# Performance work log

Measured on AMD Instinct MI355X. Metric: run time of the kernel, lower is better.

## Reference

```python
import jax, jax.numpy as jnp
import numpy as np

EMB = 256
ENT_NUM = 100000
REL_NUM = 2000
B = 512


def setup_inputs() -> dict:
    key = jax.random.key(0)
    ks = jax.random.split(key, 10)
    s = 0.02
    return {
        "left_child": jax.random.normal(ks[0], (B, 3, EMB), jnp.float32),
        "right_child": jax.random.normal(ks[1], (B, 3, EMB), jnp.float32),
        "query": jax.random.normal(ks[2], (B, 3, EMB), jnp.float32),
        "ent_emb": jax.random.normal(ks[3], (ENT_NUM, EMB), jnp.float32) * s,
        "rel_emb": jax.random.normal(ks[4], (REL_NUM, EMB), jnp.float32) * s,
        "W_left": jax.random.normal(ks[5], (EMB, EMB), jnp.float32) * s,
        "b_left": jnp.zeros((EMB,), jnp.float32),
        "W_right": jax.random.normal(ks[6], (EMB, EMB), jnp.float32) * s,
        "b_right": jnp.zeros((EMB,), jnp.float32),
        "W_ent": jax.random.normal(ks[7], (EMB, 3 * EMB), jnp.float32) * s,
        "b_ent": jnp.zeros((EMB,), jnp.float32),
    }


def _attend(q, table):
    # q: [B, E], table: [N, E]. Fused form of expand*mul*sum + softmax + expand*mul*sum.
    logits = q @ table.T                     # [B, N]
    probs = jax.nn.softmax(logits, axis=1)   # [B, N]
    return probs @ table                     # [B, E]


def reference(left_child, right_child, query, ent_emb, rel_emb,
              W_left, b_left, W_right, b_right, W_ent, b_ent):
    q1 = query[:, 1, :]
    left_rel = q1 @ W_left.T + b_left
    right_rel = q1 @ W_right.T + b_right
    # cat(query[:,0], query[:,1], query[:,2]) along dim 1 == reshape
    q_cat = query.reshape(query.shape[0], 3 * EMB)
    q_ent = q_cat @ W_ent.T + b_ent

    o_ent = _attend(q_ent, ent_emb)
    o_left_r = _attend(left_rel, rel_emb)
    o_right_r = _attend(right_rel, rel_emb)

    new_left = jnp.stack([left_child[:, 0, :], o_left_r, o_ent], axis=1)
    new_right = jnp.stack([o_ent, o_right_r, right_child[:, 2, :]], axis=1)
    return (new_left, new_right)
```

## Files before the change

kernel.cpp:

```cpp
#include <hip/hip_runtime.h>
#include <hip/hip_bf16.h>
#include <math.h>

typedef __bf16 bf16;
typedef unsigned short u16;
typedef unsigned int u32;
typedef unsigned long long u64;
typedef long long i64;
typedef unsigned char u8;
typedef __attribute__((ext_vector_type(8))) __bf16 bf16x8;
typedef __attribute__((ext_vector_type(16))) float f32x16;
typedef __attribute__((ext_vector_type(8))) int i32x8;
typedef __attribute__((address_space(1))) void gvoid;
typedef __attribute__((address_space(3))) void svoid;

#define ENT_N 100000
#define REL_N 2000
#define ENT_CH 120
#define REL_CH 4

#define NPREPM 1536
#define NCONV  6380
#define NCOPY  256

static __device__ __forceinline__ i32x8 mk8(uint4 a, uint4 b) {
    i32x8 r;
    r[0] = (int)a.x; r[1] = (int)a.y; r[2] = (int)a.z; r[3] = (int)a.w;
    r[4] = (int)b.x; r[5] = (int)b.y; r[6] = (int)b.z; r[7] = (int)b.w;
    return r;
}

template<int KLEN>
static __device__ __forceinline__ void prep_tile(
    const float* __restrict__ query, const float* __restrict__ W,
    const float* __restrict__ bias, int b0, int rowbase, int qwoff,
    bf16* __restrict__ outBf, u8* __restrict__ out8, float* smem)
{
    const int t = threadIdx.x;
    float* qs = smem;
    float* Wl = smem + 4 * KLEN;

#pragma unroll
    for (int i = 0; i < 4 * KLEN / 256; ++i) {
        const int l = t + 256 * i;
        const int r = l / KLEN, k = l % KLEN;
        qs[l] = query[(size_t)(b0 + r) * 768 + qwoff + k];
    }

    const int j = t & 63, r = t >> 6;
    float acc = 0.f;
    const float* wbase = W + (size_t)rowbase * KLEN;

    for (int c = 0; c < KLEN / 32; ++c) {
        __syncthreads();
#pragma unroll
        for (int p = 0; p < 2; ++p) {
            const int idx = t + p * 256;
            const int row = idx >> 3, kq = idx & 7;
            const float4 v = *(const float4*)(wbase + (size_t)row * KLEN + c * 32 + kq * 4);
            float* d = Wl + row * 33 + kq * 4;
            d[0] = v.x; d[1] = v.y; d[2] = v.z; d[3] = v.w;
        }
        __syncthreads();
        const float* wr = Wl + j * 33;
        const float* qr = qs + r * KLEN + c * 32;
#pragma unroll
        for (int k = 0; k < 32; ++k) acc += wr[k] * qr[k];
    }
    acc += bias[rowbase + j];

    const size_t o = (size_t)(b0 + r) * 256 + rowbase + j;
    outBf[o] = (bf16)acc;
    out8[o] = (u8)__builtin_amdgcn_cvt_pk_fp8_f32(acc, acc, 0, false);
}

__global__ __launch_bounds__(256) void prep_conv(
    const float* __restrict__ query,
    const float* __restrict__ W_left, const float* __restrict__ b_left,
    const float* __restrict__ W_right, const float* __restrict__ b_right,
    const float* __restrict__ W_ent, const float* __restrict__ b_ent,
    const float* __restrict__ lc, const float* __restrict__ rc,
    bf16* __restrict__ qe, bf16* __restrict__ ql, bf16* __restrict__ qr,
    u8* __restrict__ qe8, u8* __restrict__ ql8, u8* __restrict__ qr8,
    float* __restrict__ out,
    const float* __restrict__ entF, const float* __restrict__ relF,
    u8* __restrict__ entT, u8* __restrict__ entB,
    u8* __restrict__ relT, u8* __restrict__ relB,
    int nconv)
{
    __shared__ float smem[5184];
    const int blk = blockIdx.x;
    const int t = threadIdx.x;

    if (blk < NPREPM) {
        const int rg = blk / 12, jt = blk % 12;
        const int b0 = rg * 4;
        const int proj = jt >> 2, rowbase = (jt & 3) * 64;
        if (proj == 0)
            prep_tile<768>(query, W_ent, b_ent, b0, rowbase, 0, qe, qe8, smem);
        else if (proj == 1)
            prep_tile<256>(query, W_left, b_left, b0, rowbase, 256, ql, ql8, smem);
        else
            prep_tile<256>(query, W_right, b_right, b0, rowbase, 256, qr, qr8, smem);
        return;
    }
    if (blk >= NPREPM + nconv) {
        const int idx = (blk - NPREPM - nconv) * 256 + t;
        if (idx < 32768) {
            const int q = idx >> 6, e4 = idx & 63;
            float4 v = *(const float4*)(lc + (size_t)q * 768 + e4 * 4);
            *(float4*)(out + (size_t)q * 768 + e4 * 4) = v;
        } else {
            const int j = idx - 32768;
            const int q = j >> 6, e4 = j & 63;
            float4 v = *(const float4*)(rc + (size_t)q * 768 + 512 + e4 * 4);
            *(float4*)(out + (size_t)393216 + q * 768 + 512 + e4 * 4) = v;
        }
        return;
    }

    const int cidx = blk - NPREPM;
    const int x = cidx >> 2, y = cidx & 3;
    const float* in; u8* outT; u8* outB; int R; int g;
    if (x < 1563) {
        in = entF; outT = entT; outB = entB; R = ENT_N; g = x;
    } else {
        in = relF; outT = relT; outB = relB; R = REL_N; g = x - 1563;
    }
    const int r0 = g * 64;
    float* tile = smem;
    const int e0 = y * 64;

    const int eg = t & 7, rowb = t >> 3;
#pragma unroll
    for (int item = 0; item < 2; ++item) {
        const int r = rowb + item * 32;
        float4 a, b;
        if ((r0 + r) < R) {
            const float* src = in + (size_t)(r0 + r) * 256 + e0 + eg * 8;
            a = *(const float4*)src;
            b = *(const float4*)(src + 4);
        } else { a = make_float4(0.f, 0.f, 0.f, 0.f); b = a; }
        float* dst = tile + r * 65 + eg * 8;
        dst[0] = a.x; dst[1] = a.y; dst[2] = a.z; dst[3] = a.w;
        dst[4] = b.x; dst[5] = b.y; dst[6] = b.z; dst[7] = b.w;
    }
    __syncthreads();

    {
        const int n2 = t >> 2, piece = t & 3;
        const int sub = n2 >> 5, nn = n2 & 31;
        const int kbk = piece >> 1, jh = piece & 1;
        const float* src = tile + n2 * 65 + kbk * 32 + jh * 16;
        u32 xx; uint4 o;
        xx = __builtin_amdgcn_cvt_pk_fp8_f32(src[0], src[1], 0, false);
        o.x = __builtin_amdgcn_cvt_pk_fp8_f32(src[2], src[3], xx, true);
        xx = __builtin_amdgcn_cvt_pk_fp8_f32(src[4], src[5], 0, false);
        o.y = __builtin_amdgcn_cvt_pk_fp8_f32(src[6], src[7], xx, true);
        xx = __builtin_amdgcn_cvt_pk_fp8_f32(src[8], src[9], 0, false);
        o.z = __builtin_amdgcn_cvt_pk_fp8_f32(src[10], src[11], xx, true);
        xx = __builtin_amdgcn_cvt_pk_fp8_f32(src[12], src[13], 0, false);
        o.w = __builtin_amdgcn_cvt_pk_fp8_f32(src[14], src[15], xx, true);
        *(uint4*)(outB + (size_t)g * 16384 + sub * 8192 +
                  (size_t)y * 2048 + kbk * 1024 + nn * 32 + jh * 16) = o;
    }
    {
        const int etl = t >> 7, kbv = (t >> 6) & 1;
        const int nv = (t >> 1) & 31, jh = t & 1;
        const int colL = etl * 32 + nv;
        float v[16];
#pragma unroll
        for (int i = 0; i < 16; ++i) {
            const int row = jh * 32 + (i & 3) + 8 * (i >> 2) + 4 * kbv;
            v[i] = tile[row * 65 + colL];
        }
        u32 xx; uint4 o;
        xx = __builtin_amdgcn_cvt_pk_fp8_f32(v[0], v[1], 0, false);
        o.x = __builtin_amdgcn_cvt_pk_fp8_f32(v[2], v[3], xx, true);
        xx = __builtin_amdgcn_cvt_pk_fp8_f32(v[4], v[5], 0, false);
        o.y = __builtin_amdgcn_cvt_pk_fp8_f32(v[6], v[7], xx, true);
        xx = __builtin_amdgcn_cvt_pk_fp8_f32(v[8], v[9], 0, false);
        o.z = __builtin_amdgcn_cvt_pk_fp8_f32(v[10], v[11], xx, true);
        xx = __builtin_amdgcn_cvt_pk_fp8_f32(v[12], v[13], 0, false);
        o.w = __builtin_amdgcn_cvt_pk_fp8_f32(v[14], v[15], xx, true);
        *(uint4*)(outT + (size_t)g * 16384 +
                  (size_t)(y * 2 + etl) * 2048 +
                  kbv * 1024 + nv * 32 + jh * 16) = o;
    }
}

__global__ __launch_bounds__(256, 2) void flash10(
    const u8* __restrict__ qeP, const u8* __restrict__ qlP,
    const u8* __restrict__ qrP,
    const u8* __restrict__ entB, const u8* __restrict__ relB,
    const u8* __restrict__ entT, const u8* __restrict__ relT,
    float* __restrict__ entL, float* __restrict__ relLL,
    float* __restrict__ relLR,
    u16* __restrict__ entO, u16* __restrict__ relOL, u16* __restrict__ relOR)
{
    const int tid = threadIdx.x;
    const int w = tid >> 6;
    const int lane = tid & 63;
    const int n = lane & 31;
    const int kb = lane >> 5;

    int qt, c, stride, nt, Nrows;
    const u8* qbf; const u8* tabB; const u8* tabT;
    float* pL; u16* pO;
    {
        const int id = blockIdx.x;
        if (id < 480) {
            qt = id / 120; c = id % 120;
            stride = 120; nt = (c < 3) ? 14 : 13;
            Nrows = ENT_N;
            qbf = qeP; tabB = entB; tabT = entT; pL = entL; pO = entO;
        } else {
            const int r = id - 480;
            qt = (r >> 2) & 3; c = r & 3;
            stride = 4; nt = 8;
            Nrows = REL_N;
            tabB = relB; tabT = relT;
            if (r < 16) { qbf = qlP; pL = relLL; pO = relOL; }
            else        { qbf = qrP; pL = relLR; pO = relOR; }
        }
    }
    const int q0 = qt * 128;
    const int qw = q0 + w * 32;

    __shared__ __align__(16) u8 lds[65536];
    u16* lds16 = (u16*)lds;

    const u8* qrow = qbf + (size_t)(qw + n) * 256;
    i32x8 qf[4];
#pragma unroll
    for (int kc = 0; kc < 4; ++kc) {
        uint4 a = *(const uint4*)(qrow + kc * 64 + kb * 32);
        uint4 b = *(const uint4*)(qrow + kc * 64 + kb * 32 + 16);
        qf[kc] = mk8(a, b);
    }

    f32x16 acc[8];
#pragma unroll
    for (int et = 0; et < 8; ++et)
#pragma unroll
        for (int i = 0; i < 16; ++i) acc[et][i] = 0.f;
    float l_run = 0.f;

    auto stage = [&](int buf, int g) {
        u8* sK = lds + buf * 32768;
        u8* sV = sK + 16384;
        const u8* ksrc = tabB + (size_t)g * 16384 + w * 4096 + (size_t)lane * 16;
        const u8* vsrc = tabT + (size_t)g * 16384 + w * 4096 + (size_t)lane * 16;
#pragma unroll
        for (int o = 0; o < 4096; o += 1024) {
            __builtin_amdgcn_global_load_lds((gvoid*)(ksrc + o),
                                             (svoid*)(sK + w * 4096 + o), 16, 0, 0);
            __builtin_amdgcn_global_load_lds((gvoid*)(vsrc + o),
                                             (svoid*)(sV + w * 4096 + o), 16, 0, 0);
        }
    };

    int rt = c;
    stage(0, rt);
    __syncthreads();

    for (int k = 0; k < nt; ++k) {
        if (k + 1 < nt) stage((k + 1) & 1, rt + stride);

        const u8* sK = lds + (k & 1) * 32768;
        const u8* sV = sK + 16384;
        const int gr = rt * 64;

        f32x16 L0, L1;
#pragma unroll
        for (int i = 0; i < 16; ++i) { L0[i] = 0.f; L1[i] = 0.f; }
        const u8* kbase = sK + kb * 1024 + n * 32;
#pragma unroll
        for (int kc = 0; kc < 4; ++kc) {
            uint4 a0 = *(const uint4*)(kbase + kc * 2048);
            uint4 a1 = *(const uint4*)(kbase + kc * 2048 + 16);
            L0 = __builtin_amdgcn_mfma_scale_f32_32x32x64_f8f6f4(
                mk8(a0, a1), qf[kc], L0, 0, 0, 0, 0x7f7f7f7f, 0, 0x7f7f7f7f);
            uint4 b0 = *(const uint4*)(kbase + 8192 + kc * 2048);
            uint4 b1 = *(const uint4*)(kbase + 8192 + kc * 2048 + 16);
            L1 = __builtin_amdgcn_mfma_scale_f32_32x32x64_f8f6f4(
                mk8(b0, b1), qf[kc], L1, 0, 0, 0, 0x7f7f7f7f, 0, 0x7f7f7f7f);
        }
        if (gr + 64 > Nrows) {
#pragma unroll
            for (int r = 0; r < 16; ++r) {
                const int row = (r & 3) + 8 * (r >> 2) + 4 * kb;
                if (gr + row >= Nrows)      L0[r] = -1e30f;
                if (gr + 32 + row >= Nrows) L1[r] = -1e30f;
            }
        }
        float rs = 0.f;
#pragma unroll
        for (int r = 0; r < 16; ++r) {
            const float p0 = __expf(L0[r]); L0[r] = p0; rs += p0;
            const float p1 = __expf(L1[r]); L1[r] = p1; rs += p1;
        }
        rs += __shfl_xor(rs, 32);
        l_run += rs;
        u32 p[8];
#pragma unroll
        for (int i = 0; i < 4; ++i) {
            u32 x = __builtin_amdgcn_cvt_pk_fp8_f32(L0[i * 4 + 0], L0[i * 4 + 1], 0, false);
            p[i] = __builtin_amdgcn_cvt_pk_fp8_f32(L0[i * 4 + 2], L0[i * 4 + 3], x, true);
            u32 y = __builtin_amdgcn_cvt_pk_fp8_f32(L1[i * 4 + 0], L1[i * 4 + 1], 0, false);
            p[i + 4] = __builtin_amdgcn_cvt_pk_fp8_f32(L1[i * 4 + 2], L1[i * 4 + 3], y, true);
        }
        uint4 pa; pa.x = p[0]; pa.y = p[1]; pa.z = p[2]; pa.w = p[3];
        uint4 pb; pb.x = p[4]; pb.y = p[5]; pb.z = p[6]; pb.w = p[7];
        const i32x8 bv = mk8(pa, pb);
        const u8* vbase = sV + kb * 1024 + n * 32;
#pragma unroll
        for (int et = 0; et < 8; ++et) {
            uint4 v0 = *(const uint4*)(vbase + et * 2048);
            uint4 v1 = *(const uint4*)(vbase + et * 2048 + 16);
            acc[et] = __builtin_amdgcn_mfma_scale_f32_32x32x64_f8f6f4(
                mk8(v0, v1), bv, acc[et], 0, 0, 0, 0x7f7f7f7f, 0, 0x7f7f7f7f);
        }
        rt += stride;
        __syncthreads();
    }

    if (lane < 32) pL[(size_t)c * 512 + qw + n] = l_run;

    for (int half = 0; half < 2; ++half) {
        __syncthreads();
        if ((w >> 1) == half) {
            u16* rgn = lds16 + (w & 1) * 8448;
#pragma unroll
            for (int et = 0; et < 8; ++et)
#pragma unroll
                for (int a2 = 0; a2 < 4; ++a2) {
                    bf16 h0 = (bf16)acc[et][a2 * 4 + 0];
                    bf16 h1 = (bf16)acc[et][a2 * 4 + 1];
                    bf16 h2 = (bf16)acc[et][a2 * 4 + 2];
                    bf16 h3 = (bf16)acc[et][a2 * 4 + 3];
                    uint2 pk;
                    pk.x = ((u32)(*(u16*)&h1) << 16) | (u32)(*(u16*)&h0);
                    pk.y = ((u32)(*(u16*)&h3) << 16) | (u32)(*(u16*)&h2);
                    *(uint2*)(rgn + n * 264 + et * 32 + 8 * a2 + 4 * kb) = pk;
                }
        }
        __syncthreads();
#pragma unroll
        for (int rg = 0; rg < 2; ++rg) {
            const int qt2 = q0 + (half * 2 + rg) * 32;
            const u16* src = lds16 + rg * 8448;
            const int qq = tid >> 3, e0 = (tid & 7) * 32;
#pragma unroll
            for (int i = 0; i < 4; ++i) {
                const u16* sp = src + qq * 264 + e0 + i * 8;
                uint2 a = *(const uint2*)(sp);
                uint2 b = *(const uint2*)(sp + 4);
                uint4 wv; wv.x = a.x; wv.y = a.y; wv.z = b.x; wv.w = b.y;
                *(uint4*)(pO + ((size_t)c * 512 + qt2 + qq) * 256 + e0 + i * 8) = wv;
            }
        }
    }
}

__global__ __launch_bounds__(256) void combine_all(
    const u16* __restrict__ entO, const float* __restrict__ entL,
    const u16* __restrict__ relOL, const float* __restrict__ relLL,
    const u16* __restrict__ relOR, const float* __restrict__ relLR,
    float* __restrict__ out)
{
    const u16* pO; const float* pl; int CH, baseA, baseB;
    if (blockIdx.y == 0) { pO = entO; pl = entL; CH = ENT_CH; baseA = 512; baseB = 393216; }
    else if (blockIdx.y == 1) { pO = relOL; pl = relLL; CH = REL_CH; baseA = 256; baseB = -1; }
    else { pO = relOR; pl = relLR; CH = REL_CH; baseA = 393472; baseB = -1; }

    const int idx = blockIdx.x * 256 + threadIdx.x;
    const int q = idx >> 5;
    const int e0 = (idx & 31) * 8;
    float s = 0.f;
#pragma unroll 4
    for (int c = 0; c < CH; ++c) s += pl[(size_t)c * 512 + q];
    const float inv = 1.f / s;
    float a[8];
#pragma unroll
    for (int k = 0; k < 8; ++k) a[k] = 0.f;
#pragma unroll 4
    for (int c = 0; c < CH; ++c) {
        const uint4 wv = *(const uint4*)(pO + ((size_t)c * 512 + q) * 256 + e0);
        const u32 ww[4] = {wv.x, wv.y, wv.z, wv.w};
#pragma unroll
        for (int p = 0; p < 4; ++p) {
            a[p * 2]     += __uint_as_float((ww[p] & 0xffffu) << 16);
            a[p * 2 + 1] += __uint_as_float(ww[p] & 0xffff0000u);
        }
    }
#pragma unroll
    for (int k = 0; k < 8; ++k) a[k] *= inv;
    float4 o1 = {a[0], a[1], a[2], a[3]};
    float4 o2 = {a[4], a[5], a[6], a[7]};
    *(float4*)(out + (size_t)baseA + (size_t)q * 768 + e0) = o1;
    *(float4*)(out + (size_t)baseA + (size_t)q * 768 + e0 + 4) = o2;
    if (baseB >= 0) {
        *(float4*)(out + (size_t)baseB + (size_t)q * 768 + e0) = o1;
        *(float4*)(out + (size_t)baseB + (size_t)q * 768 + e0 + 4) = o2;
    }
}

__global__ __launch_bounds__(256) void attend_simple(
    const bf16* __restrict__ qbf, const float* __restrict__ tab, int Nrows,
    float* __restrict__ out, int baseA, int baseB)
{
    const int q = blockIdx.x;
    const int t = threadIdx.x, wave = t >> 6, lane = t & 63;
    float qv[4];
#pragma unroll
    for (int i = 0; i < 4; ++i) qv[i] = (float)qbf[(size_t)q * 256 + lane + 64 * i];
    float m = -INFINITY, l = 0.f, o[4] = {0.f, 0.f, 0.f, 0.f};
    for (int r = wave; r < Nrows; r += 4) {
        const float* row = tab + (size_t)r * 256;
        float d = 0.f;
#pragma unroll
        for (int i = 0; i < 4; ++i) d += qv[i] * row[lane + 64 * i];
#pragma unroll
        for (int s = 32; s; s >>= 1) d += __shfl_xor(d, s);
        const float mn = fmaxf(m, d);
        const float al = __expf(m - mn);
        const float p = __expf(d - mn);
#pragma unroll
        for (int i = 0; i < 4; ++i) o[i] = o[i] * al + p * row[lane + 64 * i];
        l = l * al + p; m = mn;
    }
    __shared__ float sm[4], sl[4], so[4][256];
    if (lane == 0) { sm[wave] = m; sl[wave] = l; }
#pragma unroll
    for (int i = 0; i < 4; ++i) so[wave][lane + 64 * i] = o[i];
    __syncthreads();
    const float M = fmaxf(fmaxf(sm[0], sm[1]), fmaxf(sm[2], sm[3]));
    const float w0 = __expf(sm[0] - M), w1 = __expf(sm[1] - M);
    const float w2 = __expf(sm[2] - M), w3 = __expf(sm[3] - M);
    const float L = w0 * sl[0] + w1 * sl[1] + w2 * sl[2] + w3 * sl[3];
    const float a = (w0 * so[0][t] + w1 * so[1][t] + w2 * so[2][t] + w3 * so[3][t]) / L;
    out[(size_t)baseA + (size_t)q * 768 + t] = a;
    if (baseB >= 0) out[(size_t)baseB + (size_t)q * 768 + t] = a;
}

extern "C" void kernel_launch(void* const* d_in, const int* in_sizes, int n_in,
                              void* d_out, int out_size, void* d_ws, size_t ws_size,
                              hipStream_t stream)
{
    const float* left_child  = (const float*)d_in[0];
    const float* right_child = (const float*)d_in[1];
    const float* query       = (const float*)d_in[2];
    const float* ent_emb     = (const float*)d_in[3];
    const float* rel_emb     = (const float*)d_in[4];
    const float* W_left      = (const float*)d_in[5];
    const float* b_left      = (const float*)d_in[6];
    const float* W_right     = (const float*)d_in[7];
    const float* b_right     = (const float*)d_in[8];
    const float* W_ent       = (const float*)d_in[9];
    const float* b_ent       = (const float*)d_in[10];
    float* out = (float*)d_out;
    char* ws = (char*)d_ws;

    bf16* qe_bf = (bf16*)(ws + 0);
    bf16* ql_bf = (bf16*)(ws + 262144);
    bf16* qr_bf = (bf16*)(ws + 524288);
    u8*   qe8   = (u8*)(ws + 786432);
    u8*   ql8   = (u8*)(ws + 917504);
    u8*   qr8   = (u8*)(ws + 1048576);
    u8*   entT8 = (u8*)(ws + 1179648);
    u8*   relT8 = (u8*)(ws + 26787840);
    u8*   entB8 = (u8*)(ws + 27312128);
    u8*   relB8 = (u8*)(ws + 52920320);
    float* entL = (float*)(ws + 53444608);
    u16*  entO  = (u16*)(ws + 53690368);
    float* relLL = (float*)(ws + 85147648);
    float* relLR = (float*)(ws + 85155840);
    u16*  relOL = (u16*)(ws + 85164032);
    u16*  relOR = (u16*)(ws + 86212608);
    const size_t WS_FULL = 87261184;
    const size_t WS_FALLBACK = 786432;

    if (ws_size >= WS_FULL) {
        prep_conv<<<dim3(NPREPM + NCONV + NCOPY), dim3(256), 0, stream>>>(
            query, W_left, b_left, W_right, b_right, W_ent, b_ent,
            left_child, right_child, qe_bf, ql_bf, qr_bf, qe8, ql8, qr8, out,
            ent_emb, rel_emb, entT8, entB8, relT8, relB8, NCONV);
        flash10<<<dim3(512), dim3(256), 0, stream>>>(
            qe8, ql8, qr8, entB8, relB8, entT8, relT8,
            entL, relLL, relLR, entO, relOL, relOR);
        combine_all<<<dim3(64, 3), dim3(256), 0, stream>>>(
            entO, entL, relOL, relLL, relOR, relLR, out);
    } else if (ws_size >= WS_FALLBACK) {
        prep_conv<<<dim3(NPREPM + NCOPY), dim3(256), 0, stream>>>(
            query, W_left, b_left, W_right, b_right, W_ent, b_ent,
            left_child, right_child, qe_bf, ql_bf, qr_bf, qe8, ql8, qr8, out,
            ent_emb, rel_emb, (u8*)ws, (u8*)ws, (u8*)ws, (u8*)ws, 0);
        attend_simple<<<dim3(512), dim3(256), 0, stream>>>(qe_bf, ent_emb, ENT_N, out, 512, 393216);
        attend_simple<<<dim3(512), dim3(256), 0, stream>>>(ql_bf, rel_emb, REL_N, out, 256, -1);
        attend_simple<<<dim3(512), dim3(256), 0, stream>>>(qr_bf, rel_emb, REL_N, out, 393472, -1);
    }
    (void)in_sizes; (void)n_in; (void)out_size;
}
```

Baseline: 246.9 us.

## Make conversion blocks persistent with prefetch; split combine over chunk segments

The fp8 table conversion in prep_conv now uses 1792 persistent blocks that loop over the 6380 tile items. Each block loads the next tile into registers while converting the current one from shared memory. The conversion blocks are placed first in the grid, ahead of the projection and copy blocks. combine_all now splits each output's chunk reduction across four threads and merges them through shared memory over a 4x larger grid, to raise parallelism and cut per-thread serial loads. The cost is extra barriers and shared-memory traffic, and fewer blocks left to hide latency.

```diff
diff --git a/kernel.cpp b/kernel.cpp
--- a/kernel.cpp
+++ b/kernel.cpp
@@ -20,7 +20,8 @@
 #define REL_CH 4
 
 #define NPREPM 1536
-#define NCONV  6380
+#define NITEMS 6380
+#define NCONVB 1792
 #define NCOPY  256
 
 static __device__ __forceinline__ i32x8 mk8(uint4 a, uint4 b) {
@@ -92,8 +93,9 @@
     const int blk = blockIdx.x;
     const int t = threadIdx.x;
 
-    if (blk < NPREPM) {
-        const int rg = blk / 12, jt = blk % 12;
+    if (blk >= nconv && blk < nconv + NPREPM) {
+        const int pb = blk - nconv;
+        const int rg = pb / 12, jt = pb % 12;
         const int b0 = rg * 4;
         const int proj = jt >> 2, rowbase = (jt & 3) * 64;
         if (proj == 0)
@@ -104,8 +106,8 @@
             prep_tile<256>(query, W_right, b_right, b0, rowbase, 256, qr, qr8, smem);
         return;
     }
-    if (blk >= NPREPM + nconv) {
-        const int idx = (blk - NPREPM - nconv) * 256 + t;
+    if (blk >= nconv + NPREPM) {
+        const int idx = (blk - nconv - NPREPM) * 256 + t;
         if (idx < 32768) {
             const int q = idx >> 6, e4 = idx & 63;
             float4 v = *(const float4*)(lc + (size_t)q * 768 + e4 * 4);
@@ -119,73 +121,92 @@
         return;
     }
 
-    const int cidx = blk - NPREPM;
-    const int x = cidx >> 2, y = cidx & 3;
-    const float* in; u8* outT; u8* outB; int R; int g;
-    if (x < 1563) {
-        in = entF; outT = entT; outB = entB; R = ENT_N; g = x;
-    } else {
-        in = relF; outT = relT; outB = relB; R = REL_N; g = x - 1563;
-    }
-    const int r0 = g * 64;
     float* tile = smem;
-    const int e0 = y * 64;
-
     const int eg = t & 7, rowb = t >> 3;
-#pragma unroll
-    for (int item = 0; item < 2; ++item) {
-        const int r = rowb + item * 32;
-        float4 a, b;
-        if ((r0 + r) < R) {
-            const float* src = in + (size_t)(r0 + r) * 256 + e0 + eg * 8;
-            a = *(const float4*)src;
-            b = *(const float4*)(src + 4);
-        } else { a = make_float4(0.f, 0.f, 0.f, 0.f); b = a; }
-        float* dst = tile + r * 65 + eg * 8;
-        dst[0] = a.x; dst[1] = a.y; dst[2] = a.z; dst[3] = a.w;
-        dst[4] = b.x; dst[5] = b.y; dst[6] = b.z; dst[7] = b.w;
-    }
-    __syncthreads();
-
-    {
-        const int n2 = t >> 2, piece = t & 3;
-        const int sub = n2 >> 5, nn = n2 & 31;
-        const int kbk = piece >> 1, jh = piece & 1;
-        const float* src = tile + n2 * 65 + kbk * 32 + jh * 16;
-        u32 xx; uint4 o;
-        xx = __builtin_amdgcn_cvt_pk_fp8_f32(src[0], src[1], 0, false);
-        o.x = __builtin_amdgcn_cvt_pk_fp8_f32(src[2], src[3], xx, true);
-        xx = __builtin_amdgcn_cvt_pk_fp8_f32(src[4], src[5], 0, false);
-        o.y = __builtin_amdgcn_cvt_pk_fp8_f32(src[6], src[7], xx, true);
-        xx = __builtin_amdgcn_cvt_pk_fp8_f32(src[8], src[9], 0, false);
-        o.z = __builtin_amdgcn_cvt_pk_fp8_f32(src[10], src[11], xx, true);
-        xx = __builtin_amdgcn_cvt_pk_fp8_f32(src[12], src[13], 0, false);
-        o.w = __builtin_amdgcn_cvt_pk_fp8_f32(src[14], src[15], xx, true);
-        *(uint4*)(outB + (size_t)g * 16384 + sub * 8192 +
-                  (size_t)y * 2048 + kbk * 1024 + nn * 32 + jh * 16) = o;
-    }
-    {
-        const int etl = t >> 7, kbv = (t >> 6) & 1;
-        const int nv = (t >> 1) & 31, jh = t & 1;
-        const int colL = etl * 32 + nv;
-        float v[16];
-#pragma unroll
-        for (int i = 0; i < 16; ++i) {
-            const int row = jh * 32 + (i & 3) + 8 * (i >> 2) + 4 * kbv;
-            v[i] = tile[row * 65 + colL];
-        }
-        u32 xx; uint4 o;
-        xx = __builtin_amdgcn_cvt_pk_fp8_f32(v[0], v[1], 0, false);
-        o.x = __builtin_amdgcn_cvt_pk_fp8_f32(v[2], v[3], xx, true);
-        xx = __builtin_amdgcn_cvt_pk_fp8_f32(v[4], v[5], 0, false);
-        o.y = __builtin_amdgcn_cvt_pk_fp8_f32(v[6], v[7], xx, true);
-        xx = __builtin_amdgcn_cvt_pk_fp8_f32(v[8], v[9], 0, false);
-        o.z = __builtin_amdgcn_cvt_pk_fp8_f32(v[10], v[11], xx, true);
-        xx = __builtin_amdgcn_cvt_pk_fp8_f32(v[12], v[13], 0, false);
-        o.w = __builtin_amdgcn_cvt_pk_fp8_f32(v[14], v[15], xx, true);
-        *(uint4*)(outT + (size_t)g * 16384 +
-                  (size_t)(y * 2 + etl) * 2048 +
-                  kbv * 1024 + nv * 32 + jh * 16) = o;
+
+    float4 A0, B0, A1, B1;
+
+    auto cissue = [&](int it) {
+        const int x = it >> 2, y = it & 3;
+        const float* in; int R, g;
+        if (x < 1563) { in = entF; R = ENT_N; g = x; }
+        else          { in = relF; R = REL_N; g = x - 1563; }
+        const int r0 = g * 64, e0 = y * 64;
+        const int ra = r0 + rowb, rb = r0 + rowb + 32;
+        if (ra < R) {
+            const float* s0 = in + (size_t)ra * 256 + e0 + eg * 8;
+            A0 = *(const float4*)s0; B0 = *(const float4*)(s0 + 4);
+        } else { A0 = make_float4(0.f, 0.f, 0.f, 0.f); B0 = A0; }
+        if (rb < R) {
+            const float* s1 = in + (size_t)rb * 256 + e0 + eg * 8;
+            A1 = *(const float4*)s1; B1 = *(const float4*)(s1 + 4);
+        } else { A1 = make_float4(0.f, 0.f, 0.f, 0.f); B1 = A1; }
+    };
+
+    auto cemit = [&](int it) {
+        const int x = it >> 2, y = it & 3;
+        u8* oT; u8* oB; int g;
+        if (x < 1563) { oT = entT; oB = entB; g = x; }
+        else          { oT = relT; oB = relB; g = x - 1563; }
+        {
+            const int n2 = t >> 2, piece = t & 3;
+            const int sub = n2 >> 5, nn = n2 & 31;
+            const int kbk = piece >> 1, jh = piece & 1;
+            const float* src = tile + n2 * 65 + kbk * 32 + jh * 16;
+            u32 xx; uint4 o;
+            xx = __builtin_amdgcn_cvt_pk_fp8_f32(src[0], src[1], 0, false);
+            o.x = __builtin_amdgcn_cvt_pk_fp8_f32(src[2], src[3], xx, true);
+            xx = __builtin_amdgcn_cvt_pk_fp8_f32(src[4], src[5], 0, false);
+            o.y = __builtin_amdgcn_cvt_pk_fp8_f32(src[6], src[7], xx, true);
+            xx = __builtin_amdgcn_cvt_pk_fp8_f32(src[8], src[9], 0, false);
+            o.z = __builtin_amdgcn_cvt_pk_fp8_f32(src[10], src[11], xx, true);
+            xx = __builtin_amdgcn_cvt_pk_fp8_f32(src[12], src[13], 0, false);
+            o.w = __builtin_amdgcn_cvt_pk_fp8_f32(src[14], src[15], xx, true);
+            *(uint4*)(oB + (size_t)g * 16384 + sub * 8192 +
+                      (size_t)y * 2048 + kbk * 1024 + nn * 32 + jh * 16) = o;
+        }
+        {
+            const int etl = t >> 7, kbv = (t >> 6) & 1;
+            const int nv = (t >> 1) & 31, jh = t & 1;
+            const int colL = etl * 32 + nv;
+            float v[16];
+#pragma unroll
+            for (int i = 0; i < 16; ++i) {
+                const int row = jh * 32 + (i & 3) + 8 * (i >> 2) + 4 * kbv;
+                v[i] = tile[row * 65 + colL];
+            }
+            u32 xx; uint4 o;
+            xx = __builtin_amdgcn_cvt_pk_fp8_f32(v[0], v[1], 0, false);
+            o.x = __builtin_amdgcn_cvt_pk_fp8_f32(v[2], v[3], xx, true);
+            xx = __builtin_amdgcn_cvt_pk_fp8_f32(v[4], v[5], 0, false);
+            o.y = __builtin_amdgcn_cvt_pk_fp8_f32(v[6], v[7], xx, true);
+            xx = __builtin_amdgcn_cvt_pk_fp8_f32(v[8], v[9], 0, false);
+            o.z = __builtin_amdgcn_cvt_pk_fp8_f32(v[10], v[11], xx, true);
+            xx = __builtin_amdgcn_cvt_pk_fp8_f32(v[12], v[13], 0, false);
+            o.w = __builtin_amdgcn_cvt_pk_fp8_f32(v[14], v[15], xx, true);
+            *(uint4*)(oT + (size_t)g * 16384 +
+                      (size_t)(y * 2 + etl) * 2048 +
+                      kbv * 1024 + nv * 32 + jh * 16) = o;
+        }
+    };
+
+    int it = blk;
+    cissue(it);
+    while (it < NITEMS) {
+        const int nxt = it + NCONVB;
+        __syncthreads();
+        {
+            float* d0 = tile + rowb * 65 + eg * 8;
+            d0[0] = A0.x; d0[1] = A0.y; d0[2] = A0.z; d0[3] = A0.w;
+            d0[4] = B0.x; d0[5] = B0.y; d0[6] = B0.z; d0[7] = B0.w;
+            float* d1 = tile + (rowb + 32) * 65 + eg * 8;
+            d1[0] = A1.x; d1[1] = A1.y; d1[2] = A1.z; d1[3] = A1.w;
+            d1[4] = B1.x; d1[5] = B1.y; d1[6] = B1.z; d1[7] = B1.w;
+        }
+        if (nxt < NITEMS) cissue(nxt);
+        __syncthreads();
+        cemit(it);
+        it = nxt;
     }
 }
 
@@ -374,18 +395,22 @@
     else if (blockIdx.y == 1) { pO = relOL; pl = relLL; CH = REL_CH; baseA = 256; baseB = -1; }
     else { pO = relOR; pl = relLR; CH = REL_CH; baseA = 393472; baseB = -1; }
 
-    const int idx = blockIdx.x * 256 + threadIdx.x;
-    const int q = idx >> 5;
-    const int e0 = (idx & 31) * 8;
+    const int t = threadIdx.x;
+    const int qi = t >> 7;
+    const int e0g = (t >> 2) & 31;
+    const int seg = t & 3;
+    const int q = blockIdx.x * 2 + qi;
+    const int e0 = e0g * 8;
+    const int cnt = CH >> 2;
+    const int cbeg = seg * cnt;
+
     float s = 0.f;
-#pragma unroll 4
-    for (int c = 0; c < CH; ++c) s += pl[(size_t)c * 512 + q];
-    const float inv = 1.f / s;
     float a[8];
 #pragma unroll
     for (int k = 0; k < 8; ++k) a[k] = 0.f;
-#pragma unroll 4
-    for (int c = 0; c < CH; ++c) {
+#pragma unroll 6
+    for (int c = cbeg; c < cbeg + cnt; ++c) {
+        s += pl[(size_t)c * 512 + q];
         const uint4 wv = *(const uint4*)(pO + ((size_t)c * 512 + q) * 256 + e0);
         const u32 ww[4] = {wv.x, wv.y, wv.z, wv.w};
 #pragma unroll
@@ -394,15 +419,36 @@
             a[p * 2 + 1] += __uint_as_float(ww[p] & 0xffff0000u);
         }
     }
-#pragma unroll
-    for (int k = 0; k < 8; ++k) a[k] *= inv;
-    float4 o1 = {a[0], a[1], a[2], a[3]};
-    float4 o2 = {a[4], a[5], a[6], a[7]};
-    *(float4*)(out + (size_t)baseA + (size_t)q * 768 + e0) = o1;
-    *(float4*)(out + (size_t)baseA + (size_t)q * 768 + e0 + 4) = o2;
-    if (baseB >= 0) {
-        *(float4*)(out + (size_t)baseB + (size_t)q * 768 + e0) = o1;
-        *(float4*)(out + (size_t)baseB + (size_t)q * 768 + e0 + 4) = o2;
+
+    __shared__ float red[2][32][4][11];
+    float* slot = red[qi][e0g][seg];
+#pragma unroll
+    for (int k = 0; k < 8; ++k) slot[k] = a[k];
+    slot[8] = s;
+    __syncthreads();
+    if (seg == 0) {
+        float st = 0.f;
+        float b[8];
+#pragma unroll
+        for (int k = 0; k < 8; ++k) b[k] = 0.f;
+#pragma unroll
+        for (int sgi = 0; sgi < 4; ++sgi) {
+            const float* sl = red[qi][e0g][sgi];
+            st += sl[8];
+#pragma unroll
+            for (int k = 0; k < 8; ++k) b[k] += sl[k];
+        }
+        const float inv = 1.f / st;
+#pragma unroll
+        for (int k = 0; k < 8; ++k) b[k] *= inv;
+        float4 o1 = {b[0], b[1], b[2], b[3]};
+        float4 o2 = {b[4], b[5], b[6], b[7]};
+        *(float4*)(out + (size_t)baseA + (size_t)q * 768 + e0) = o1;
+        *(float4*)(out + (size_t)baseA + (size_t)q * 768 + e0 + 4) = o2;
+        if (baseB >= 0) {
+            *(float4*)(out + (size_t)baseB + (size_t)q * 768 + e0) = o1;
+            *(float4*)(out + (size_t)baseB + (size_t)q * 768 + e0 + 4) = o2;
+        }
     }
 }
 
@@ -482,14 +528,14 @@
     const size_t WS_FALLBACK = 786432;
 
     if (ws_size >= WS_FULL) {
-        prep_conv<<<dim3(NPREPM + NCONV + NCOPY), dim3(256), 0, stream>>>(
+        prep_conv<<<dim3(NCONVB + NPREPM + NCOPY), dim3(256), 0, stream>>>(
             query, W_left, b_left, W_right, b_right, W_ent, b_ent,
             left_child, right_child, qe_bf, ql_bf, qr_bf, qe8, ql8, qr8, out,
-            ent_emb, rel_emb, entT8, entB8, relT8, relB8, NCONV);
+            ent_emb, rel_emb, entT8, entB8, relT8, relB8, NCONVB);
         flash10<<<dim3(512), dim3(256), 0, stream>>>(
             qe8, ql8, qr8, entB8, relB8, entT8, relT8,
             entL, relLL, relLR, entO, relOL, relOR);
-        combine_all<<<dim3(64, 3), dim3(256), 0, stream>>>(
+        combine_all<<<dim3(256, 3), dim3(256), 0, stream>>>(
             entO, entL, relOL, relLL, relOR, relLR, out);
     } else if (ws_size >= WS_FALLBACK) {
         prep_conv<<<dim3(NPREPM + NCOPY), dim3(256), 0, stream>>>(
```

After: 252.1 us. 2.1% more time.

## Double-buffer weight tiles in prep and split combine reduction across threads

Applied to the files above, without the earlier changes.

The projection tile loader in prep now prefetches the next 32-column weight chunk into registers while computing on the current chunk. It ping-pongs between two LDS buffers, which removes one barrier per iteration and raises the shared allocation. The combine kernel now splits the chunk reduction across four threads per output vector and merges the partials through shared memory. It launches 4x more blocks, meant to expose more parallelism and memory-level concurrency on the 120-chunk entity reduction. A macro is renamed as well.

```diff
diff --git a/kernel.cpp b/kernel.cpp
--- a/kernel.cpp
+++ b/kernel.cpp
@@ -20,7 +20,7 @@
 #define REL_CH 4
 
 #define NPREPM 1536
-#define NCONV  6380
+#define NITEMS 6380
 #define NCOPY  256
 
 static __device__ __forceinline__ i32x8 mk8(uint4 a, uint4 b) {
@@ -48,24 +48,33 @@
     }
 
     const int j = t & 63, r = t >> 6;
+    const int srow = t >> 3, skq = t & 7;
+    const float* wbase = W + (size_t)rowbase * KLEN;
+
+    float4 v0, v1;
+    auto wload = [&](int c) {
+        v0 = *(const float4*)(wbase + (size_t)srow * KLEN + c * 32 + skq * 4);
+        v1 = *(const float4*)(wbase + (size_t)(srow + 32) * KLEN + c * 32 + skq * 4);
+    };
+    auto wstore = [&](float* dst) {
+        float* d0 = dst + srow * 33 + skq * 4;
+        d0[0] = v0.x; d0[1] = v0.y; d0[2] = v0.z; d0[3] = v0.w;
+        float* d1 = dst + (srow + 32) * 33 + skq * 4;
+        d1[0] = v1.x; d1[1] = v1.y; d1[2] = v1.z; d1[3] = v1.w;
+    };
+
     float acc = 0.f;
-    const float* wbase = W + (size_t)rowbase * KLEN;
-
-    for (int c = 0; c < KLEN / 32; ++c) {
+    wload(0);
+    wstore(Wl);
+    constexpr int NC = KLEN / 32;
+    for (int c = 0; c < NC; ++c) {
+        if (c + 1 < NC) wload(c + 1);
         __syncthreads();
-#pragma unroll
-        for (int p = 0; p < 2; ++p) {
-            const int idx = t + p * 256;
-            const int row = idx >> 3, kq = idx & 7;
-            const float4 v = *(const float4*)(wbase + (size_t)row * KLEN + c * 32 + kq * 4);
-            float* d = Wl + row * 33 + kq * 4;
-            d[0] = v.x; d[1] = v.y; d[2] = v.z; d[3] = v.w;
-        }
-        __syncthreads();
-        const float* wr = Wl + j * 33;
+        const float* wr = Wl + (c & 1) * 2112 + j * 33;
         const float* qr = qs + r * KLEN + c * 32;
 #pragma unroll
         for (int k = 0; k < 32; ++k) acc += wr[k] * qr[k];
+        if (c + 1 < NC) wstore(Wl + ((c + 1) & 1) * 2112);
     }
     acc += bias[rowbase + j];
 
@@ -88,7 +97,7 @@
     u8* __restrict__ relT, u8* __restrict__ relB,
     int nconv)
 {
-    __shared__ float smem[5184];
+    __shared__ float smem[7296];
     const int blk = blockIdx.x;
     const int t = threadIdx.x;
 
@@ -374,18 +383,22 @@
     else if (blockIdx.y == 1) { pO = relOL; pl = relLL; CH = REL_CH; baseA = 256; baseB = -1; }
     else { pO = relOR; pl = relLR; CH = REL_CH; baseA = 393472; baseB = -1; }
 
-    const int idx = blockIdx.x * 256 + threadIdx.x;
-    const int q = idx >> 5;
-    const int e0 = (idx & 31) * 8;
+    const int t = threadIdx.x;
+    const int qi = t >> 7;
+    const int e0g = (t >> 2) & 31;
+    const int seg = t & 3;
+    const int q = blockIdx.x * 2 + qi;
+    const int e0 = e0g * 8;
+    const int cnt = CH >> 2;
+    const int cbeg = seg * cnt;
+
     float s = 0.f;
-#pragma unroll 4
-    for (int c = 0; c < CH; ++c) s += pl[(size_t)c * 512 + q];
-    const float inv = 1.f / s;
     float a[8];
 #pragma unroll
     for (int k = 0; k < 8; ++k) a[k] = 0.f;
-#pragma unroll 4
-    for (int c = 0; c < CH; ++c) {
+#pragma unroll 6
+    for (int c = cbeg; c < cbeg + cnt; ++c) {
+        s += pl[(size_t)c * 512 + q];
         const uint4 wv = *(const uint4*)(pO + ((size_t)c * 512 + q) * 256 + e0);
         const u32 ww[4] = {wv.x, wv.y, wv.z, wv.w};
 #pragma unroll
@@ -394,15 +407,36 @@
             a[p * 2 + 1] += __uint_as_float(ww[p] & 0xffff0000u);
         }
     }
-#pragma unroll
-    for (int k = 0; k < 8; ++k) a[k] *= inv;
-    float4 o1 = {a[0], a[1], a[2], a[3]};
-    float4 o2 = {a[4], a[5], a[6], a[7]};
-    *(float4*)(out + (size_t)baseA + (size_t)q * 768 + e0) = o1;
-    *(float4*)(out + (size_t)baseA + (size_t)q * 768 + e0 + 4) = o2;
-    if (baseB >= 0) {
-        *(float4*)(out + (size_t)baseB + (size_t)q * 768 + e0) = o1;
-        *(float4*)(out + (size_t)baseB + (size_t)q * 768 + e0 + 4) = o2;
+
+    __shared__ float red[2][32][4][11];
+    float* slot = red[qi][e0g][seg];
+#pragma unroll
+    for (int k = 0; k < 8; ++k) slot[k] = a[k];
+    slot[8] = s;
+    __syncthreads();
+    if (seg == 0) {
+        float st = 0.f;
+        float b[8];
+#pragma unroll
+        for (int k = 0; k < 8; ++k) b[k] = 0.f;
+#pragma unroll
+        for (int sgi = 0; sgi < 4; ++sgi) {
+            const float* sl = red[qi][e0g][sgi];
+            st += sl[8];
+#pragma unroll
+            for (int k = 0; k < 8; ++k) b[k] += sl[k];
+        }
+        const float inv = 1.f / st;
+#pragma unroll
+        for (int k = 0; k < 8; ++k) b[k] *= inv;
+        float4 o1 = {b[0], b[1], b[2], b[3]};
+        float4 o2 = {b[4], b[5], b[6], b[7]};
+        *(float4*)(out + (size_t)baseA + (size_t)q * 768 + e0) = o1;
+        *(float4*)(out + (size_t)baseA + (size_t)q * 768 + e0 + 4) = o2;
+        if (baseB >= 0) {
+            *(float4*)(out + (size_t)baseB + (size_t)q * 768 + e0) = o1;
+            *(float4*)(out + (size_t)baseB + (size_t)q * 768 + e0 + 4) = o2;
+        }
     }
 }
 
@@ -482,14 +516,14 @@
     const size_t WS_FALLBACK = 786432;
 
     if (ws_size >= WS_FULL) {
-        prep_conv<<<dim3(NPREPM + NCONV + NCOPY), dim3(256), 0, stream>>>(
+        prep_conv<<<dim3(NPREPM + NITEMS + NCOPY), dim3(256), 0, stream>>>(
             query, W_left, b_left, W_right, b_right, W_ent, b_ent,
             left_child, right_child, qe_bf, ql_bf, qr_bf, qe8, ql8, qr8, out,
-            ent_emb, rel_emb, entT8, entB8, relT8, relB8, NCONV);
+            ent_emb, rel_emb, entT8, entB8, relT8, relB8, NITEMS);
         flash10<<<dim3(512), dim3(256), 0, stream>>>(
             qe8, ql8, qr8, entB8, relB8, entT8, relT8,
             entL, relLL, relLR, entO, relOL, relOR);
-        combine_all<<<dim3(64, 3), dim3(256), 0, stream>>>(
+        combine_all<<<dim3(256, 3), dim3(256), 0, stream>>>(
             entO, entL, relOL, relLL, relOR, relLR, out);
     } else if (ws_size >= WS_FALLBACK) {
         prep_conv<<<dim3(NPREPM + NCOPY), dim3(256), 0, stream>>>(
```

New measurement: 236.8 us. 1.04x faster.
